# Optimization experiments

Measured on AMD Instinct MI355X. Metric: run time of the kernel, lower is better.

Reference implementation:

```python
import jax, jax.numpy as jnp
from jax import lax
import numpy as np

T, B, D, H = 4096, 8, 512, 512


def sru_layer(x, W, b, c0):
    # x: [T,B,D], W: [3H,D], b: [2H], c0: [B,H]
    U = jnp.einsum('tbd,hd->tbh', x, W)          # [T,B,3H] fused projection
    x_tilde, f_pre, r_pre = jnp.split(U, 3, axis=-1)
    f = jax.nn.sigmoid(f_pre + b[:H])            # forget gate [T,B,H]
    r = jax.nn.sigmoid(r_pre + b[H:])            # reset gate  [T,B,H]

    def step(c, inp):
        xt, ft = inp
        c_new = ft * c + (1.0 - ft) * xt         # elementwise recurrence
        return c_new, c_new

    c_last, cs = lax.scan(step, c0, (x_tilde, f))
    h = r * jnp.tanh(cs) + (1.0 - r) * x         # highway connection
    return h, c_last


def setup_inputs() -> dict:
    key = jax.random.key(0)
    k0, k1, k2 = jax.random.split(key, 3)
    scale = 1.0 / np.sqrt(D)
    return {
        'x': jax.random.normal(k0, (T, B, D), dtype=jnp.float32),
        'W0': jax.random.normal(k1, (3 * H, D), dtype=jnp.float32) * scale,
        'b0': jnp.zeros((2 * H,), dtype=jnp.float32),
        'W1': jax.random.normal(k2, (3 * H, H), dtype=jnp.float32) * scale,
        'b1': jnp.zeros((2 * H,), dtype=jnp.float32),
    }


def reference(x, W0, b0, W1, b1):
    c0 = jnp.zeros((x.shape[1], H), dtype=x.dtype)
    h, c = sru_layer(x, W0, b0, c0)
    h, c = sru_layer(h, W1, b1, c0)   # original resets c0 each layer
    return h, c
```

## Files before the change

### kernel.cpp

```cpp
#include <hip/hip_runtime.h>
#include <hip/hip_bf16.h>


#define T_DIM 4096
#define B_DIM 8
#define H_DIM 512
#define M_DIM (T_DIM * B_DIM)
#define N3H 1536
#define K_DIM 512
#define NCHUNK 256
#define CLEN (T_DIM / NCHUNK)
#define NCHAIN (B_DIM * H_DIM)

typedef __attribute__((ext_vector_type(8))) short s16x8;
typedef __attribute__((ext_vector_type(4))) float f32x4;
typedef unsigned short ushort_t;
typedef unsigned int uint_t;

__device__ __forceinline__ float bf2f(ushort_t u) {
    return __uint_as_float(((uint_t)u) << 16);
}
__device__ __forceinline__ ushort_t f2bf(float f) {
    uint_t u = __float_as_uint(f);
    u += 0x7FFFu + ((u >> 16) & 1u);
    return (ushort_t)(u >> 16);
}
__device__ __forceinline__ float sigm(float z) {
    return 1.0f / (1.0f + __expf(-z));
}
__device__ __forceinline__ float tanh_fast(float z) {
    float e = __expf(2.0f * z);
    return (e - 1.0f) / (e + 1.0f);
}

__global__ void cvt_f32_bf16(const float* __restrict__ in, ushort_t* __restrict__ out, int n4) {
    int i = blockIdx.x * blockDim.x + threadIdx.x;
    if (i < n4) {
        float4 v = reinterpret_cast<const float4*>(in)[i];
        ushort4 o;
        o.x = f2bf(v.x); o.y = f2bf(v.y); o.z = f2bf(v.z); o.w = f2bf(v.w);
        reinterpret_cast<ushort4*>(out)[i] = o;
    }
}

__global__ void gemm_bt(const ushort_t* __restrict__ A, const ushort_t* __restrict__ Bm,
                        ushort_t* __restrict__ C, int M, int N, int K) {
    __shared__ ushort_t As[128 * 64];
    __shared__ ushort_t Bs[128 * 64];
    const int ntn = N >> 7;
    const int nwg = gridDim.x;
    const int bid = (int)blockIdx.x;
    const int id = (bid & 7) * (nwg >> 3) + (bid >> 3);
    const int tm = id / ntn;
    const int tn = id % ntn;
    const int row0 = tm << 7, col0 = tn << 7;
    const int tid = threadIdx.x;
    const int wave = tid >> 6, lane = tid & 63;
    const int frow = (wave >> 1) << 6;
    const int fcol = (wave & 1) << 6;
    f32x4 acc[4][4] = {};

    const int lr = lane >> 3;
    const int lc = (lane & 7) << 3;

    for (int k0 = 0; k0 < K; k0 += 64) {
#pragma unroll
        for (int i = 0; i < 4; ++i) {
            const int r = i * 32 + wave * 8;
            const ushort_t* ga = A + (size_t)(row0 + r + lr) * K + k0 + lc;
            const ushort_t* gb = Bm + (size_t)(col0 + r + lr) * K + k0 + lc;
            __builtin_amdgcn_global_load_lds(
                (const __attribute__((address_space(1))) void*)ga,
                (__attribute__((address_space(3))) void*)&As[r * 64], 16, 0, 0);
            __builtin_amdgcn_global_load_lds(
                (const __attribute__((address_space(1))) void*)gb,
                (__attribute__((address_space(3))) void*)&Bs[r * 64], 16, 0, 0);
        }
        __syncthreads();
#pragma unroll
        for (int kk = 0; kk < 64; kk += 32) {
            const int kb = kk + ((lane >> 4) << 3);
            s16x8 af[4], bfr[4];
#pragma unroll
            for (int m = 0; m < 4; ++m)
                af[m] = *reinterpret_cast<const s16x8*>(&As[(frow + m * 16 + (lane & 15)) * 64 + kb]);
#pragma unroll
            for (int n = 0; n < 4; ++n)
                bfr[n] = *reinterpret_cast<const s16x8*>(&Bs[(fcol + n * 16 + (lane & 15)) * 64 + kb]);
#pragma unroll
            for (int m = 0; m < 4; ++m)
#pragma unroll
                for (int n = 0; n < 4; ++n)
                    acc[m][n] = __builtin_amdgcn_mfma_f32_16x16x32_bf16(af[m], bfr[n], acc[m][n], 0, 0, 0);
        }
        __syncthreads();
    }
    const int crow = (lane >> 4) << 2;
    const int ccol = lane & 15;
#pragma unroll
    for (int m = 0; m < 4; ++m)
#pragma unroll
        for (int n = 0; n < 4; ++n)
#pragma unroll
            for (int v = 0; v < 4; ++v)
                C[(size_t)(row0 + frow + m * 16 + crow + v) * N + (col0 + fcol + n * 16 + ccol)] =
                    f2bf(acc[m][n][v]);
}

__global__ void scan_summary(const ushort_t* __restrict__ U, const float* __restrict__ bias,
                             float* __restrict__ Sa, float* __restrict__ Sb) {
    const int b = blockIdx.x / NCHUNK;
    const int chunk = blockIdx.x % NCHUNK;
    const int h = threadIdx.x << 2;
    float fb[4];
#pragma unroll
    for (int j = 0; j < 4; ++j) fb[j] = bias[h + j];
    float Aa[4] = {1.f, 1.f, 1.f, 1.f};
    float Bb[4] = {0.f, 0.f, 0.f, 0.f};
    const ushort_t* rp = U + ((size_t)(chunk * CLEN) * B_DIM + b) * N3H + h;
    ushort4 xt = *reinterpret_cast<const ushort4*>(rp);
    ushort4 fp = *reinterpret_cast<const ushort4*>(rp + H_DIM);
#pragma unroll
    for (int s = 0; s < CLEN; ++s) {
        ushort4 xt_n, fp_n;
        if (s + 1 < CLEN) {
            rp += (size_t)B_DIM * N3H;
            xt_n = *reinterpret_cast<const ushort4*>(rp);
            fp_n = *reinterpret_cast<const ushort4*>(rp + H_DIM);
        }
        float xs[4] = {bf2f(xt.x), bf2f(xt.y), bf2f(xt.z), bf2f(xt.w)};
        float fs[4] = {bf2f(fp.x), bf2f(fp.y), bf2f(fp.z), bf2f(fp.w)};
#pragma unroll
        for (int j = 0; j < 4; ++j) {
            float f = sigm(fs[j] + fb[j]);
            Aa[j] *= f;
            Bb[j] = f * Bb[j] + (1.f - f) * xs[j];
        }
        xt = xt_n; fp = fp_n;
    }
    const int cb = chunk * NCHAIN + b * H_DIM + h;
#pragma unroll
    for (int j = 0; j < 4; ++j) { Sa[cb + j] = Aa[j]; Sb[cb + j] = Bb[j]; }
}

__global__ void scan_fixup(float* Sa, const float* Sb, float* __restrict__ clast) {
    const int chain = blockIdx.x * blockDim.x + threadIdx.x;
    float c = 0.f;
    float a = Sa[chain];
    float bv = Sb[chain];
#pragma unroll 4
    for (int k = 0; k < NCHUNK; ++k) {
        float a_n = 0.f, b_n = 0.f;
        if (k + 1 < NCHUNK) {
            a_n = Sa[(k + 1) * NCHAIN + chain];
            b_n = Sb[(k + 1) * NCHAIN + chain];
        }
        Sa[k * NCHAIN + chain] = c;
        c = a * c + bv;
        a = a_n; bv = b_n;
    }
    if (clast) clast[chain] = c;
}

template <bool IN_BF16, bool OUT_BF16>
__global__ void scan_apply(const ushort_t* __restrict__ U, const float* __restrict__ bias,
                           const float* __restrict__ centry,
                           const void* __restrict__ xin, void* __restrict__ hout) {
    const int b = blockIdx.x / NCHUNK;
    const int chunk = blockIdx.x % NCHUNK;
    const int h = threadIdx.x << 2;
    const int cb = chunk * NCHAIN + b * H_DIM + h;
    float cc[4], fb[4], rb[4];
#pragma unroll
    for (int j = 0; j < 4; ++j) {
        cc[j] = centry[cb + j];
        fb[j] = bias[h + j];
        rb[j] = bias[H_DIM + h + j];
    }
    size_t row = (size_t)(chunk * CLEN) * B_DIM + b;
    const ushort_t* rp = U + row * N3H + h;
    size_t xoff = row * H_DIM + h;

    ushort4 xt = *reinterpret_cast<const ushort4*>(rp);
    ushort4 fp = *reinterpret_cast<const ushort4*>(rp + H_DIM);
    ushort4 rr = *reinterpret_cast<const ushort4*>(rp + 2 * H_DIM);
    float xv[4];
    if (IN_BF16) {
        ushort4 xi = *reinterpret_cast<const ushort4*>((const ushort_t*)xin + xoff);
        xv[0] = bf2f(xi.x); xv[1] = bf2f(xi.y); xv[2] = bf2f(xi.z); xv[3] = bf2f(xi.w);
    } else {
        float4 xi = *reinterpret_cast<const float4*>((const float*)xin + xoff);
        xv[0] = xi.x; xv[1] = xi.y; xv[2] = xi.z; xv[3] = xi.w;
    }

#pragma unroll
    for (int s = 0; s < CLEN; ++s) {
        ushort4 xt_n, fp_n, rr_n;
        float xv_n[4];
        if (s + 1 < CLEN) {
            rp += (size_t)B_DIM * N3H;
            xt_n = *reinterpret_cast<const ushort4*>(rp);
            fp_n = *reinterpret_cast<const ushort4*>(rp + H_DIM);
            rr_n = *reinterpret_cast<const ushort4*>(rp + 2 * H_DIM);
            size_t xo2 = xoff + (size_t)B_DIM * H_DIM;
            if (IN_BF16) {
                ushort4 xi = *reinterpret_cast<const ushort4*>((const ushort_t*)xin + xo2);
                xv_n[0] = bf2f(xi.x); xv_n[1] = bf2f(xi.y); xv_n[2] = bf2f(xi.z); xv_n[3] = bf2f(xi.w);
            } else {
                float4 xi = *reinterpret_cast<const float4*>((const float*)xin + xo2);
                xv_n[0] = xi.x; xv_n[1] = xi.y; xv_n[2] = xi.z; xv_n[3] = xi.w;
            }
        }
        float xts[4] = {bf2f(xt.x), bf2f(xt.y), bf2f(xt.z), bf2f(xt.w)};
        float fps[4] = {bf2f(fp.x), bf2f(fp.y), bf2f(fp.z), bf2f(fp.w)};
        float rps[4] = {bf2f(rr.x), bf2f(rr.y), bf2f(rr.z), bf2f(rr.w)};
        float hv[4];
#pragma unroll
        for (int j = 0; j < 4; ++j) {
            float f = sigm(fps[j] + fb[j]);
            cc[j] = f * cc[j] + (1.f - f) * xts[j];
            float r = sigm(rps[j] + rb[j]);
            hv[j] = r * tanh_fast(cc[j]) + (1.f - r) * xv[j];
        }
        if (OUT_BF16) {
            ushort4 o;
            o.x = f2bf(hv[0]); o.y = f2bf(hv[1]); o.z = f2bf(hv[2]); o.w = f2bf(hv[3]);
            *reinterpret_cast<ushort4*>((ushort_t*)hout + xoff) = o;
        } else {
            float4 o;
            o.x = hv[0]; o.y = hv[1]; o.z = hv[2]; o.w = hv[3];
            *reinterpret_cast<float4*>((float*)hout + xoff) = o;
        }
        xoff += (size_t)B_DIM * H_DIM;
        xt = xt_n; fp = fp_n; rr = rr_n;
        xv[0] = xv_n[0]; xv[1] = xv_n[1]; xv[2] = xv_n[2]; xv[3] = xv_n[3];
    }
}

extern "C" void kernel_launch(void* const* d_in, const int* in_sizes, int n_in,
                              void* d_out, int out_size, void* d_ws, size_t ws_size,
                              hipStream_t stream) {
    (void)in_sizes; (void)n_in; (void)out_size; (void)ws_size;
    const float* x  = (const float*)d_in[0];
    const float* W0 = (const float*)d_in[1];
    const float* b0 = (const float*)d_in[2];
    const float* W1 = (const float*)d_in[3];
    const float* b1 = (const float*)d_in[4];
    float* out = (float*)d_out;

    char* ws = (char*)d_ws;
    ushort_t* xb  = (ushort_t*)(ws);
    float*    Sa  = (float*)(ws);
    float*    Sb  = (float*)(ws + 4194304);
    ushort_t* h1  = (ushort_t*)(ws + 33554432);
    ushort_t* W0b = (ushort_t*)(ws + 67108864);
    ushort_t* W1b = (ushort_t*)(ws + 68681728);
    ushort_t* U   = (ushort_t*)(ws + 70254592);

    cvt_f32_bf16<<<(M_DIM * K_DIM / 4 + 255) / 256, 256, 0, stream>>>(x, xb, M_DIM * K_DIM / 4);
    cvt_f32_bf16<<<(N3H * K_DIM / 4 + 255) / 256, 256, 0, stream>>>(W0, W0b, N3H * K_DIM / 4);
    cvt_f32_bf16<<<(N3H * K_DIM / 4 + 255) / 256, 256, 0, stream>>>(W1, W1b, N3H * K_DIM / 4);

    const int gemm_grid = (M_DIM / 128) * (N3H / 128);
    const int scan_grid = B_DIM * NCHUNK;

    gemm_bt<<<gemm_grid, 256, 0, stream>>>(xb, W0b, U, M_DIM, N3H, K_DIM);
    scan_summary<<<scan_grid, 128, 0, stream>>>(U, b0, Sa, Sb);
    scan_fixup<<<NCHAIN / 256, 256, 0, stream>>>(Sa, Sb, nullptr);
    scan_apply<false, true><<<scan_grid, 128, 0, stream>>>(U, b0, Sa, (const void*)x, (void*)h1);

    gemm_bt<<<gemm_grid, 256, 0, stream>>>(h1, W1b, U, M_DIM, N3H, K_DIM);
    scan_summary<<<scan_grid, 128, 0, stream>>>(U, b1, Sa, Sb);
    scan_fixup<<<NCHAIN / 256, 256, 0, stream>>>(Sa, Sb, out + (size_t)M_DIM * H_DIM);
    scan_apply<true, false><<<scan_grid, 128, 0, stream>>>(U, b1, Sa, (const void*)h1, (void*)out);
}
```

Measured before the change: 336.7 us.

## Use 256x256 double-buffered swizzled GEMM, hierarchical scan fixup, fused conversions

Replaces the 128x128 GEMM with a 256x256 tile, 512-thread kernel that double-buffers LDS, XOR-swizzles the LDS layout against bank conflicts, and interleaves MFMA phases with barriers and setprio. The single serial 256-step scan fixup becomes a two-level scan: 16 groups run in parallel, then a 16-step pass, and scan_apply combines the local prefix with the group entry value. The three fp32-to-bf16 conversion launches are merged into one. The aim is fewer launches, a shorter serial fixup chain and better GEMM data reuse, at the cost of 128 KB of LDS per block and lower occupancy.

```diff
diff --git a/kernel.cpp b/kernel.cpp
--- a/kernel.cpp
+++ b/kernel.cpp
@@ -11,6 +11,8 @@
 #define NCHUNK 256
 #define CLEN (T_DIM / NCHUNK)
 #define NCHAIN (B_DIM * H_DIM)
+#define NGRP 16
+#define GLEN (NCHUNK / NGRP)
 
 typedef __attribute__((ext_vector_type(8))) short s16x8;
 typedef __attribute__((ext_vector_type(4))) float f32x4;
@@ -33,77 +35,161 @@
     return (e - 1.0f) / (e + 1.0f);
 }
 
-__global__ void cvt_f32_bf16(const float* __restrict__ in, ushort_t* __restrict__ out, int n4) {
+#define XF4 (M_DIM * K_DIM / 4)
+#define WF4 (N3H * K_DIM / 4)
+__global__ void cvt_all(const float* __restrict__ x, const float* __restrict__ w0,
+                        const float* __restrict__ w1, ushort_t* __restrict__ xb,
+                        ushort_t* __restrict__ w0b, ushort_t* __restrict__ w1b) {
     int i = blockIdx.x * blockDim.x + threadIdx.x;
-    if (i < n4) {
-        float4 v = reinterpret_cast<const float4*>(in)[i];
-        ushort4 o;
-        o.x = f2bf(v.x); o.y = f2bf(v.y); o.z = f2bf(v.z); o.w = f2bf(v.w);
-        reinterpret_cast<ushort4*>(out)[i] = o;
-    }
-}
-
-__global__ void gemm_bt(const ushort_t* __restrict__ A, const ushort_t* __restrict__ Bm,
-                        ushort_t* __restrict__ C, int M, int N, int K) {
-    __shared__ ushort_t As[128 * 64];
-    __shared__ ushort_t Bs[128 * 64];
-    const int ntn = N >> 7;
+    const float* src; ushort_t* dst; int idx;
+    if (i < XF4) { src = x; dst = xb; idx = i; }
+    else if (i < XF4 + WF4) { src = w0; dst = w0b; idx = i - XF4; }
+    else if (i < XF4 + 2 * WF4) { src = w1; dst = w1b; idx = i - XF4 - WF4; }
+    else return;
+    float4 v = reinterpret_cast<const float4*>(src)[idx];
+    ushort4 o;
+    o.x = f2bf(v.x); o.y = f2bf(v.y); o.z = f2bf(v.z); o.w = f2bf(v.w);
+    reinterpret_cast<ushort4*>(dst)[idx] = o;
+}
+
+__device__ __forceinline__ s16x8 lds_swz_read(const ushort_t* base, int row, int kb) {
+    int byte = (row << 7) + (((kb << 1)) ^ ((row & 7) << 4));
+    return *reinterpret_cast<const s16x8*>(reinterpret_cast<const char*>(base) + byte);
+}
+
+__global__ __launch_bounds__(512) void gemm_bt256(const ushort_t* __restrict__ A,
+                                                  const ushort_t* __restrict__ Bm,
+                                                  ushort_t* __restrict__ C,
+                                                  int M, int N, int K) {
+    __shared__ ushort_t As[2][256 * 64];
+    __shared__ ushort_t Bs[2][256 * 64];
+    const int ntn = N >> 8;
     const int nwg = gridDim.x;
     const int bid = (int)blockIdx.x;
     const int id = (bid & 7) * (nwg >> 3) + (bid >> 3);
-    const int tm = id / ntn;
-    const int tn = id % ntn;
-    const int row0 = tm << 7, col0 = tn << 7;
+    const int tm = id / ntn, tn = id % ntn;
+    const int row0 = tm << 8, col0 = tn << 8;
     const int tid = threadIdx.x;
-    const int wave = tid >> 6, lane = tid & 63;
-    const int frow = (wave >> 1) << 6;
-    const int fcol = (wave & 1) << 6;
-    f32x4 acc[4][4] = {};
-
-    const int lr = lane >> 3;
-    const int lc = (lane & 7) << 3;
-
-    for (int k0 = 0; k0 < K; k0 += 64) {
-#pragma unroll
-        for (int i = 0; i < 4; ++i) {
-            const int r = i * 32 + wave * 8;
-            const ushort_t* ga = A + (size_t)(row0 + r + lr) * K + k0 + lc;
-            const ushort_t* gb = Bm + (size_t)(col0 + r + lr) * K + k0 + lc;
-            __builtin_amdgcn_global_load_lds(
-                (const __attribute__((address_space(1))) void*)ga,
-                (__attribute__((address_space(3))) void*)&As[r * 64], 16, 0, 0);
-            __builtin_amdgcn_global_load_lds(
-                (const __attribute__((address_space(1))) void*)gb,
-                (__attribute__((address_space(3))) void*)&Bs[r * 64], 16, 0, 0);
-        }
-        __syncthreads();
-#pragma unroll
-        for (int kk = 0; kk < 64; kk += 32) {
-            const int kb = kk + ((lane >> 4) << 3);
-            s16x8 af[4], bfr[4];
-#pragma unroll
-            for (int m = 0; m < 4; ++m)
-                af[m] = *reinterpret_cast<const s16x8*>(&As[(frow + m * 16 + (lane & 15)) * 64 + kb]);
-#pragma unroll
-            for (int n = 0; n < 4; ++n)
-                bfr[n] = *reinterpret_cast<const s16x8*>(&Bs[(fcol + n * 16 + (lane & 15)) * 64 + kb]);
-#pragma unroll
-            for (int m = 0; m < 4; ++m)
-#pragma unroll
-                for (int n = 0; n < 4; ++n)
-                    acc[m][n] = __builtin_amdgcn_mfma_f32_16x16x32_bf16(af[m], bfr[n], acc[m][n], 0, 0, 0);
-        }
-        __syncthreads();
-    }
+    const int wv = tid >> 6, lane = tid & 63;
+    const int wm = wv >> 2, wn = wv & 3;
+    const int l15 = lane & 15;
+    const int kgrp = (lane >> 4) << 3;
+
+    f32x4 acc[8][4] = {};
+
+    const int srow_in_wave = lane >> 3;
+    const int sslot = lane & 7;
+
+#define STAGE(buf_, t_)                                                                  \
+    {                                                                                    \
+        const int k0s = (t_) * 64;                                                       \
+        _Pragma("unroll")                                                                \
+        for (int j = 0; j < 4; ++j) {                                                    \
+            const int rl = j * 64 + wv * 8;                                              \
+            const int rme = rl + srow_in_wave;                                           \
+            const int sl = sslot ^ (rme & 7);             \
+            const ushort_t* ga = A + (size_t)(row0 + rme) * K + k0s + (sl << 3);         \
+            const ushort_t* gb = Bm + (size_t)(col0 + rme) * K + k0s + (sl << 3);        \
+            __builtin_amdgcn_global_load_lds(                                            \
+                (const __attribute__((address_space(1))) void*)ga,                       \
+                (__attribute__((address_space(3))) void*)&As[buf_][rl * 64], 16, 0, 0);  \
+            __builtin_amdgcn_global_load_lds(                                            \
+                (const __attribute__((address_space(1))) void*)gb,                       \
+                (__attribute__((address_space(3))) void*)&Bs[buf_][rl * 64], 16, 0, 0);  \
+        }                                                                                \
+    }
+
+    STAGE(0, 0);
+    asm volatile("s_waitcnt vmcnt(0)" ::: "memory");
+    __builtin_amdgcn_s_barrier();
+
+    const int nkt = K >> 6;
+    for (int t = 0; t < nkt; ++t) {
+        const int buf = t & 1;
+        const ushort_t* Ab = &As[buf][0];
+        const ushort_t* Bb = &Bs[buf][0];
+        if (t + 1 < nkt) STAGE(buf ^ 1, t + 1);
+
+        s16x8 af[4][2], bfr[4][2];
+#pragma unroll
+        for (int j = 0; j < 4; ++j)
+#pragma unroll
+            for (int kk2 = 0; kk2 < 2; ++kk2)
+                af[j][kk2] = lds_swz_read(Ab, wm * 128 + j * 16 + l15, kk2 * 32 + kgrp);
+#pragma unroll
+        for (int n = 0; n < 2; ++n)
+#pragma unroll
+            for (int kk2 = 0; kk2 < 2; ++kk2)
+                bfr[n][kk2] = lds_swz_read(Bb, wn * 64 + n * 16 + l15, kk2 * 32 + kgrp);
+        __builtin_amdgcn_s_barrier();
+        __builtin_amdgcn_s_setprio(1);
+#pragma unroll
+        for (int j = 0; j < 4; ++j)
+#pragma unroll
+            for (int n = 0; n < 2; ++n)
+#pragma unroll
+                for (int kk2 = 0; kk2 < 2; ++kk2)
+                    acc[j][n] = __builtin_amdgcn_mfma_f32_16x16x32_bf16(af[j][kk2], bfr[n][kk2], acc[j][n], 0, 0, 0);
+        __builtin_amdgcn_s_setprio(0);
+        __builtin_amdgcn_s_barrier();
+
+#pragma unroll
+        for (int n = 2; n < 4; ++n)
+#pragma unroll
+            for (int kk2 = 0; kk2 < 2; ++kk2)
+                bfr[n][kk2] = lds_swz_read(Bb, wn * 64 + n * 16 + l15, kk2 * 32 + kgrp);
+        __builtin_amdgcn_s_barrier();
+        __builtin_amdgcn_s_setprio(1);
+#pragma unroll
+        for (int j = 0; j < 4; ++j)
+#pragma unroll
+            for (int n = 2; n < 4; ++n)
+#pragma unroll
+                for (int kk2 = 0; kk2 < 2; ++kk2)
+                    acc[j][n] = __builtin_amdgcn_mfma_f32_16x16x32_bf16(af[j][kk2], bfr[n][kk2], acc[j][n], 0, 0, 0);
+        __builtin_amdgcn_s_setprio(0);
+        __builtin_amdgcn_s_barrier();
+
+#pragma unroll
+        for (int j = 0; j < 4; ++j)
+#pragma unroll
+            for (int kk2 = 0; kk2 < 2; ++kk2)
+                af[j][kk2] = lds_swz_read(Ab, wm * 128 + (4 + j) * 16 + l15, kk2 * 32 + kgrp);
+        __builtin_amdgcn_s_barrier();
+        __builtin_amdgcn_s_setprio(1);
+#pragma unroll
+        for (int j = 0; j < 4; ++j)
+#pragma unroll
+            for (int n = 0; n < 2; ++n)
+#pragma unroll
+                for (int kk2 = 0; kk2 < 2; ++kk2)
+                    acc[4 + j][n] = __builtin_amdgcn_mfma_f32_16x16x32_bf16(af[j][kk2], bfr[n][kk2], acc[4 + j][n], 0, 0, 0);
+        __builtin_amdgcn_s_setprio(0);
+        __builtin_amdgcn_s_barrier();
+
+        __builtin_amdgcn_s_setprio(1);
+#pragma unroll
+        for (int j = 0; j < 4; ++j)
+#pragma unroll
+            for (int n = 2; n < 4; ++n)
+#pragma unroll
+                for (int kk2 = 0; kk2 < 2; ++kk2)
+                    acc[4 + j][n] = __builtin_amdgcn_mfma_f32_16x16x32_bf16(af[j][kk2], bfr[n][kk2], acc[4 + j][n], 0, 0, 0);
+        __builtin_amdgcn_s_setprio(0);
+
+        asm volatile("s_waitcnt vmcnt(0)" ::: "memory");
+        __builtin_amdgcn_s_barrier();
+    }
+#undef STAGE
+
     const int crow = (lane >> 4) << 2;
-    const int ccol = lane & 15;
-#pragma unroll
-    for (int m = 0; m < 4; ++m)
+#pragma unroll
+    for (int m = 0; m < 8; ++m)
 #pragma unroll
         for (int n = 0; n < 4; ++n)
 #pragma unroll
             for (int v = 0; v < 4; ++v)
-                C[(size_t)(row0 + frow + m * 16 + crow + v) * N + (col0 + fcol + n * 16 + ccol)] =
+                C[(size_t)(row0 + wm * 128 + m * 16 + crow + v) * N + (col0 + wn * 64 + n * 16 + l15)] =
                     f2bf(acc[m][n][v]);
 }
 
@@ -143,37 +229,53 @@
     for (int j = 0; j < 4; ++j) { Sa[cb + j] = Aa[j]; Sb[cb + j] = Bb[j]; }
 }
 
-__global__ void scan_fixup(float* Sa, const float* Sb, float* __restrict__ clast) {
+__global__ void scan_fixup1(float* Sa, float* Sb, float* __restrict__ Ga, float* __restrict__ Gb) {
+    const int idx = blockIdx.x * blockDim.x + threadIdx.x;
+    const int chain = idx & (NCHAIN - 1);
+    const int g = idx >> 12;
+    float A = 1.f, B = 0.f;
+#pragma unroll
+    for (int i = 0; i < GLEN; ++i) {
+        const size_t off = (size_t)(g * GLEN + i) * NCHAIN + chain;
+        float a = Sa[off], b = Sb[off];
+        Sa[off] = A; Sb[off] = B;
+        B = a * B + b;
+        A = a * A;
+    }
+    Ga[g * NCHAIN + chain] = A;
+    Gb[g * NCHAIN + chain] = B;
+}
+
+__global__ void scan_fixup2(const float* __restrict__ Ga, const float* __restrict__ Gb,
+                            float* __restrict__ Eg, float* __restrict__ clast) {
     const int chain = blockIdx.x * blockDim.x + threadIdx.x;
     float c = 0.f;
-    float a = Sa[chain];
-    float bv = Sb[chain];
-#pragma unroll 4
-    for (int k = 0; k < NCHUNK; ++k) {
-        float a_n = 0.f, b_n = 0.f;
-        if (k + 1 < NCHUNK) {
-            a_n = Sa[(k + 1) * NCHAIN + chain];
-            b_n = Sb[(k + 1) * NCHAIN + chain];
-        }
-        Sa[k * NCHAIN + chain] = c;
-        c = a * c + bv;
-        a = a_n; bv = b_n;
+#pragma unroll
+    for (int g = 0; g < NGRP; ++g) {
+        Eg[g * NCHAIN + chain] = c;
+        c = Ga[g * NCHAIN + chain] * c + Gb[g * NCHAIN + chain];
     }
     if (clast) clast[chain] = c;
 }
 
 template <bool IN_BF16, bool OUT_BF16>
 __global__ void scan_apply(const ushort_t* __restrict__ U, const float* __restrict__ bias,
-                           const float* __restrict__ centry,
+                           const float* __restrict__ Sa, const float* __restrict__ Sb,
+                           const float* __restrict__ Eg,
                            const void* __restrict__ xin, void* __restrict__ hout) {
     const int b = blockIdx.x / NCHUNK;
     const int chunk = blockIdx.x % NCHUNK;
     const int h = threadIdx.x << 2;
     const int cb = chunk * NCHAIN + b * H_DIM + h;
+    const int eb = (chunk >> 4) * NCHAIN + b * H_DIM + h;
     float cc[4], fb[4], rb[4];
+    float4 la = *reinterpret_cast<const float4*>(&Sa[cb]);
+    float4 lb = *reinterpret_cast<const float4*>(&Sb[cb]);
+    float4 eg = *reinterpret_cast<const float4*>(&Eg[eb]);
+    cc[0] = lb.x + la.x * eg.x; cc[1] = lb.y + la.y * eg.y;
+    cc[2] = lb.z + la.z * eg.z; cc[3] = lb.w + la.w * eg.w;
 #pragma unroll
     for (int j = 0; j < 4; ++j) {
-        cc[j] = centry[cb + j];
         fb[j] = bias[h + j];
         rb[j] = bias[H_DIM + h + j];
     }
@@ -252,25 +354,29 @@
     ushort_t* xb  = (ushort_t*)(ws);
     float*    Sa  = (float*)(ws);
     float*    Sb  = (float*)(ws + 4194304);
+    float*    Ga  = (float*)(ws + 8388608);
+    float*    Gb  = (float*)(ws + 8650752);
+    float*    Eg  = (float*)(ws + 8912896);
     ushort_t* h1  = (ushort_t*)(ws + 33554432);
     ushort_t* W0b = (ushort_t*)(ws + 67108864);
     ushort_t* W1b = (ushort_t*)(ws + 68681728);
     ushort_t* U   = (ushort_t*)(ws + 70254592);
 
-    cvt_f32_bf16<<<(M_DIM * K_DIM / 4 + 255) / 256, 256, 0, stream>>>(x, xb, M_DIM * K_DIM / 4);
-    cvt_f32_bf16<<<(N3H * K_DIM / 4 + 255) / 256, 256, 0, stream>>>(W0, W0b, N3H * K_DIM / 4);
-    cvt_f32_bf16<<<(N3H * K_DIM / 4 + 255) / 256, 256, 0, stream>>>(W1, W1b, N3H * K_DIM / 4);
-
-    const int gemm_grid = (M_DIM / 128) * (N3H / 128);
+    const int cvt_total = XF4 + 2 * WF4;
+    cvt_all<<<(cvt_total + 255) / 256, 256, 0, stream>>>(x, W0, W1, xb, W0b, W1b);
+
+    const int gemm_grid = (M_DIM / 256) * (N3H / 256);
     const int scan_grid = B_DIM * NCHUNK;
 
-    gemm_bt<<<gemm_grid, 256, 0, stream>>>(xb, W0b, U, M_DIM, N3H, K_DIM);
+    gemm_bt256<<<gemm_grid, 512, 0, stream>>>(xb, W0b, U, M_DIM, N3H, K_DIM);
     scan_summary<<<scan_grid, 128, 0, stream>>>(U, b0, Sa, Sb);
-    scan_fixup<<<NCHAIN / 256, 256, 0, stream>>>(Sa, Sb, nullptr);
-    scan_apply<false, true><<<scan_grid, 128, 0, stream>>>(U, b0, Sa, (const void*)x, (void*)h1);
-
-    gemm_bt<<<gemm_grid, 256, 0, stream>>>(h1, W1b, U, M_DIM, N3H, K_DIM);
+    scan_fixup1<<<NGRP * NCHAIN / 256, 256, 0, stream>>>(Sa, Sb, Ga, Gb);
+    scan_fixup2<<<NCHAIN / 256, 256, 0, stream>>>(Ga, Gb, Eg, nullptr);
+    scan_apply<false, true><<<scan_grid, 128, 0, stream>>>(U, b0, Sa, Sb, Eg, (const void*)x, (void*)h1);
+
+    gemm_bt256<<<gemm_grid, 512, 0, stream>>>(h1, W1b, U, M_DIM, N3H, K_DIM);
     scan_summary<<<scan_grid, 128, 0, stream>>>(U, b1, Sa, Sb);
-    scan_fixup<<<NCHAIN / 256, 256, 0, stream>>>(Sa, Sb, out + (size_t)M_DIM * H_DIM);
-    scan_apply<true, false><<<scan_grid, 128, 0, stream>>>(U, b1, Sa, (const void*)h1, (void*)out);
-}
+    scan_fixup1<<<NGRP * NCHAIN / 256, 256, 0, stream>>>(Sa, Sb, Ga, Gb);
+    scan_fixup2<<<NCHAIN / 256, 256, 0, stream>>>(Ga, Gb, Eg, out + (size_t)M_DIM * H_DIM);
+    scan_apply<true, false><<<scan_grid, 128, 0, stream>>>(U, b1, Sa, Sb, Eg, (const void*)h1, (void*)out);
+}
```

New measurement: 288.7 us. -14.2%, faster.
